# Performance work log

Measured on AMD Instinct MI355X. Metric: run time of the kernel, lower is better.

Reference implementation:

```python
import jax, jax.numpy as jnp
import numpy as np

N, E_RAW, F_IN, H, C = 50000, 800000, 500, 5, 32
HID = H * C  # 160
NEG_GAT = 0.2   # GATConv leaky_relu slope for attention logits
NEG = 0.01      # F.leaky_relu default slope
LN_EPS = 1e-5


def glorot(key, shape):
    fan_in, fan_out = shape[0], shape[-1]
    lim = jnp.sqrt(6.0 / (fan_in + fan_out))
    return jax.random.uniform(key, shape, jnp.float32, -lim, lim)


def setup_inputs() -> dict:
    key = jax.random.key(0)
    ks = jax.random.split(key, 12)
    x = jax.random.normal(ks[0], (N, F_IN), jnp.float32)
    edge_index = jax.random.randint(ks[1], (2, E_RAW), 0, N, jnp.int64)
    return {
        "x": x,
        "edge_index": edge_index,
        "W1": glorot(ks[2], (F_IN, HID)),
        "att1_s": glorot(ks[3], (H, C)),
        "att1_d": glorot(ks[4], (H, C)),
        "b1": jnp.zeros((HID,), jnp.float32),
        "g1": jnp.ones((HID,), jnp.float32),
        "be1": jnp.zeros((HID,), jnp.float32),
        "W2": glorot(ks[5], (HID, HID)),
        "att2_s": glorot(ks[6], (H, C)),
        "att2_d": glorot(ks[7], (H, C)),
        "b2": jnp.zeros((HID,), jnp.float32),
        "Wm": glorot(ks[8], (HID, HID)),
        "bm": jnp.zeros((HID,), jnp.float32),
    }


def add_self_loops(edge_index):
    loops = jnp.arange(N, dtype=edge_index.dtype)
    return jnp.concatenate([edge_index, jnp.stack([loops, loops])], axis=1)


def gat_conv(x, src, dst, W, att_s, att_d, bias):
    # x: [N, Fin] -> per-head transform [N, H, C]
    xl = (x @ W).reshape(N, H, C)
    a_s = jnp.einsum('nhc,hc->nh', xl, att_s)  # [N, H]
    a_d = jnp.einsum('nhc,hc->nh', xl, att_d)
    logits = jax.nn.leaky_relu(a_s[src] + a_d[dst], NEG_GAT)  # [E, H]
    # segment softmax over incoming edges of each dst node
    lmax = jax.ops.segment_max(logits, dst, num_segments=N)
    alpha = jnp.exp(logits - lmax[dst])
    denom = jax.ops.segment_sum(alpha, dst, num_segments=N)
    alpha = alpha / (denom[dst] + 1e-16)
    msg = xl[src] * alpha[:, :, None]  # [E, H, C]
    out = jax.ops.segment_sum(msg, dst, num_segments=N)
    return out.reshape(N, HID) + bias, alpha


def layer_norm(x, g, b):
    mu = jnp.mean(x, axis=-1, keepdims=True)
    var = jnp.mean((x - mu) ** 2, axis=-1, keepdims=True)
    return (x - mu) * jax.lax.rsqrt(var + LN_EPS) * g + b


def reference(x, edge_index, W1, att1_s, att1_d, b1, g1, be1,
              W2, att2_s, att2_d, b2, Wm, bm):
    ei = add_self_loops(edge_index)
    src, dst = ei[0], ei[1]
    h, alpha1 = gat_conv(x, src, dst, W1, att1_s, att1_d, b1)
    h = jax.nn.leaky_relu(h, NEG)
    h = layer_norm(h, g1, be1)  # dropout is identity in eval mode
    h, alpha2 = gat_conv(h, src, dst, W2, att2_s, att2_d, b2)
    h = jax.nn.leaky_relu(h, NEG)
    out = jax.nn.leaky_relu(h @ Wm + bm, NEG)
    return out, alpha1, alpha2
```

## Files before the change

### kernel.cpp

```cpp
#include <hip/hip_runtime.h>

#define N_NODES 50000
#define E_RAW_N 800000
#define E_TOT   850000
#define F_IN_K  500
#define HID     160

using short8 = __attribute__((ext_vector_type(8))) short;
using f32x4  = __attribute__((ext_vector_type(4))) float;

__device__ __forceinline__ float b2f(unsigned short u) {
  union { unsigned int i; float f; } v; v.i = ((unsigned int)u) << 16; return v.f;
}
__device__ __forceinline__ unsigned short f2b(float f) {
  union { float f; unsigned int i; } v; v.f = f;
  unsigned int i = v.i;
  unsigned int lsb = (i >> 16) & 1u;
  i += 0x7fffu + lsb;
  return (unsigned short)(i >> 16);
}

__device__ __forceinline__ float wsum(float x) {
  #pragma unroll
  for (int o = 32; o; o >>= 1) x += __shfl_xor(x, o, 64);
  return x;
}
__device__ __forceinline__ float wmax(float x) {
  #pragma unroll
  for (int o = 32; o; o >>= 1) x = fmaxf(x, __shfl_xor(x, o, 64));
  return x;
}
__device__ __forceinline__ float lrelu2(float x) { return x > 0.f ? x : 0.2f * x; }

__global__ void detect_kernel(const int* __restrict__ ei, int* __restrict__ flag) {
  if (threadIdx.x == 0 && blockIdx.x == 0) {
    int allz = 1;
    for (int i = 1; i < 128; i += 2) if (ei[i] != 0) { allz = 0; break; }
    *flag = allz;
  }
}
__device__ __forceinline__ int edge_src(const int* ei, int wide, int e) {
  return wide ? ei[2 * e] : ei[e];
}
__device__ __forceinline__ int edge_dst(const int* ei, int wide, int e) {
  return wide ? ei[2 * (E_RAW_N + e)] : ei[E_RAW_N + e];
}

__global__ __launch_bounds__(256) void convert_B(const float* __restrict__ B,
                                                 unsigned short* __restrict__ Bt,
                                                 int K, int KPAD) {
  const int i = blockIdx.x * 256 + threadIdx.x;
  if (i >= HID * KPAD) return;
  const int c = i / KPAD, k = i % KPAD;
  const float b = (k < K) ? B[(long)k * HID + c] : 0.f;
  const unsigned short hi = f2b(b);
  Bt[i] = hi;
  Bt[HID * KPAD + i] = f2b(b - b2f(hi));
}

template<int K, int KPAD, int BK, int MODE, int SPLIT>
__global__ __launch_bounds__(256) void gemm_lds(
    const float* __restrict__ A, const unsigned short* __restrict__ Bt,
    float* __restrict__ C, unsigned short* __restrict__ Ch,
    const float* __restrict__ bias,
    const float* __restrict__ att_s, const float* __restrict__ att_d,
    float* __restrict__ a_s, float* __restrict__ a_d)
{
  constexpr int NP = SPLIT ? 2 : 1;
  constexpr int LSTR = BK + 8;
  constexpr int CHUNKS = KPAD / BK;
  constexpr int KSC = BK / 32;
  constexpr int ROWU = BK / 8;
  constexpr int UNITS = NP * HID * ROWU;
  __shared__ __align__(16) unsigned short Bs[NP][HID][LSTR];

  const int t = threadIdx.x;
  const int l = t & 63;
  const int w = t >> 6;
  const int m = l & 15;
  const int kgrp = (l >> 4) * 8;
  const int rbase = blockIdx.x * 64 + w * 16;
  const int arow = (rbase + m < N_NODES) ? rbase + m : N_NODES - 1;
  const float* Arow = A + (long)arow * K;

  f32x4 acc[10];
  #pragma unroll
  for (int i = 0; i < 10; ++i) acc[i] = (f32x4){0.f, 0.f, 0.f, 0.f};

  if constexpr (CHUNKS == 1) {
    float ar[KSC][8];
    #pragma unroll
    for (int ks = 0; ks < KSC; ++ks) {
      const int kb = ks * 32 + kgrp;
      if (kb + 8 <= K) {
        const float4 a0 = *(const float4*)(Arow + kb);
        const float4 a1 = *(const float4*)(Arow + kb + 4);
        ar[ks][0]=a0.x; ar[ks][1]=a0.y; ar[ks][2]=a0.z; ar[ks][3]=a0.w;
        ar[ks][4]=a1.x; ar[ks][5]=a1.y; ar[ks][6]=a1.z; ar[ks][7]=a1.w;
      } else {
        #pragma unroll
        for (int j = 0; j < 8; ++j) ar[ks][j] = (kb + j < K) ? Arow[kb + j] : 0.f;
      }
    }
    for (int u = t; u < UNITS; u += 256) {
      const int p = u / (HID * ROWU);
      const int rem = u % (HID * ROWU);
      const int c = rem / ROWU;
      const int k8 = rem % ROWU;
      const short8 v = *(const short8*)(Bt + (long)p * HID * KPAD + (long)c * KPAD + k8 * 8);
      *(short8*)&Bs[p][c][k8 * 8] = v;
    }
    __syncthreads();
    #pragma unroll
    for (int ks = 0; ks < KSC; ++ks) {
      short8 ah, al;
      #pragma unroll
      for (int j = 0; j < 8; ++j) {
        const unsigned short h = f2b(ar[ks][j]);
        ah[j] = (short)h;
        if (SPLIT) al[j] = (short)f2b(ar[ks][j] - b2f(h));
      }
      #pragma unroll
      for (int ct = 0; ct < 10; ++ct) {
        const short8 bh = *(const short8*)&Bs[0][ct * 16 + m][ks * 32 + kgrp];
        acc[ct] = __builtin_amdgcn_mfma_f32_16x16x32_bf16(ah, bh, acc[ct], 0, 0, 0);
        if (SPLIT) {
          const short8 bl = *(const short8*)&Bs[SPLIT][ct * 16 + m][ks * 32 + kgrp];
          acc[ct] = __builtin_amdgcn_mfma_f32_16x16x32_bf16(ah, bl, acc[ct], 0, 0, 0);
          acc[ct] = __builtin_amdgcn_mfma_f32_16x16x32_bf16(al, bh, acc[ct], 0, 0, 0);
        }
      }
    }
  } else {
    static_assert(UNITS % 256 == 0, "units must tile threads");
    constexpr int UPT = UNITS / 256;
    short8 rb[UPT];
    float ar[KSC][8];

    #pragma unroll
    for (int i = 0; i < UPT; ++i) {
      const int u = i * 256 + t;
      const int p = u / (HID * ROWU);
      const int rem = u % (HID * ROWU);
      const int c = rem / ROWU;
      const int k8 = rem % ROWU;
      rb[i] = *(const short8*)(Bt + (long)p * HID * KPAD + (long)c * KPAD + k8 * 8);
    }
    #pragma unroll
    for (int ks = 0; ks < KSC; ++ks) {
      const int kb = ks * 32 + kgrp;
      const float4 a0 = *(const float4*)(Arow + kb);
      const float4 a1 = *(const float4*)(Arow + kb + 4);
      ar[ks][0]=a0.x; ar[ks][1]=a0.y; ar[ks][2]=a0.z; ar[ks][3]=a0.w;
      ar[ks][4]=a1.x; ar[ks][5]=a1.y; ar[ks][6]=a1.z; ar[ks][7]=a1.w;
    }

    for (int cc = 0; cc < CHUNKS; ++cc) {
      __syncthreads();
      #pragma unroll
      for (int i = 0; i < UPT; ++i) {
        const int u = i * 256 + t;
        const int p = u / (HID * ROWU);
        const int rem = u % (HID * ROWU);
        const int c = rem / ROWU;
        const int k8 = rem % ROWU;
        *(short8*)&Bs[p][c][k8 * 8] = rb[i];
      }
      __syncthreads();
      short8 rb2[UPT];
      float ar2[KSC][8];
      if (cc + 1 < CHUNKS) {
        #pragma unroll
        for (int i = 0; i < UPT; ++i) {
          const int u = i * 256 + t;
          const int p = u / (HID * ROWU);
          const int rem = u % (HID * ROWU);
          const int c = rem / ROWU;
          const int k8 = rem % ROWU;
          rb2[i] = *(const short8*)(Bt + (long)p * HID * KPAD + (long)c * KPAD + (cc + 1) * BK + k8 * 8);
        }
        #pragma unroll
        for (int ks = 0; ks < KSC; ++ks) {
          const int kb = (cc + 1) * BK + ks * 32 + kgrp;
          if (kb + 8 <= K) {
            const float4 a0 = *(const float4*)(Arow + kb);
            const float4 a1 = *(const float4*)(Arow + kb + 4);
            ar2[ks][0]=a0.x; ar2[ks][1]=a0.y; ar2[ks][2]=a0.z; ar2[ks][3]=a0.w;
            ar2[ks][4]=a1.x; ar2[ks][5]=a1.y; ar2[ks][6]=a1.z; ar2[ks][7]=a1.w;
          } else {
            #pragma unroll
            for (int j = 0; j < 8; ++j) ar2[ks][j] = (kb + j < K) ? Arow[kb + j] : 0.f;
          }
        }
        __builtin_amdgcn_sched_barrier(0);
      }
      #pragma unroll
      for (int ks = 0; ks < KSC; ++ks) {
        short8 ah, al;
        #pragma unroll
        for (int j = 0; j < 8; ++j) {
          const unsigned short h = f2b(ar[ks][j]);
          ah[j] = (short)h;
          if (SPLIT) al[j] = (short)f2b(ar[ks][j] - b2f(h));
        }
        #pragma unroll
        for (int ct = 0; ct < 10; ++ct) {
          const short8 bh = *(const short8*)&Bs[0][ct * 16 + m][ks * 32 + kgrp];
          acc[ct] = __builtin_amdgcn_mfma_f32_16x16x32_bf16(ah, bh, acc[ct], 0, 0, 0);
          if (SPLIT) {
            const short8 bl = *(const short8*)&Bs[SPLIT][ct * 16 + m][ks * 32 + kgrp];
            acc[ct] = __builtin_amdgcn_mfma_f32_16x16x32_bf16(ah, bl, acc[ct], 0, 0, 0);
            acc[ct] = __builtin_amdgcn_mfma_f32_16x16x32_bf16(al, bh, acc[ct], 0, 0, 0);
          }
        }
      }
      if (cc + 1 < CHUNKS) {
        #pragma unroll
        for (int i = 0; i < UPT; ++i) rb[i] = rb2[i];
        #pragma unroll
        for (int ks = 0; ks < KSC; ++ks)
          #pragma unroll
          for (int j = 0; j < 8; ++j) ar[ks][j] = ar2[ks][j];
      }
    }
  }

  const int crow0 = rbase + (l >> 4) * 4;

  if (MODE == 2) {
    #pragma unroll
    for (int r = 0; r < 4; ++r) {
      float ps[5], pd[5];
      #pragma unroll
      for (int h = 0; h < 5; ++h) {
        float s = acc[2*h][r]     * att_s[(2*h) * 16 + m]
                + acc[2*h + 1][r] * att_s[(2*h + 1) * 16 + m];
        float d = acc[2*h][r]     * att_d[(2*h) * 16 + m]
                + acc[2*h + 1][r] * att_d[(2*h + 1) * 16 + m];
        #pragma unroll
        for (int o = 1; o < 16; o <<= 1) {
          s += __shfl_xor(s, o, 64);
          d += __shfl_xor(d, o, 64);
        }
        ps[h] = s; pd[h] = d;
      }
      const int crow = crow0 + r;
      if (crow < N_NODES && m < 5) {
        const float vs = m == 0 ? ps[0] : m == 1 ? ps[1] : m == 2 ? ps[2] : m == 3 ? ps[3] : ps[4];
        const float vd = m == 0 ? pd[0] : m == 1 ? pd[1] : m == 2 ? pd[2] : m == 3 ? pd[3] : pd[4];
        a_s[crow * 5 + m] = vs;
        a_d[crow * 5 + m] = vd;
      }
    }
  }

  #pragma unroll
  for (int r = 0; r < 4; ++r) {
    const int crow = crow0 + r;
    if (crow < N_NODES) {
      #pragma unroll
      for (int ct = 0; ct < 10; ++ct) {
        const int col = ct * 16 + m;
        float v = acc[ct][r];
        if (MODE == 1) { v += bias[col]; v = v > 0.f ? v : 0.01f * v; }
        if (MODE == 2) Ch[(long)crow * HID + col] = f2b(v);
        else           C[(long)crow * HID + col] = v;
      }
    }
  }
}

__global__ __launch_bounds__(256) void count_kernel(const int* __restrict__ ei,
    const int* __restrict__ flag, int* __restrict__ deg) {
  const int e = blockIdx.x * 256 + threadIdx.x;
  if (e >= E_TOT) return;
  const int wide = *flag;
  const int d = (e < E_RAW_N) ? edge_dst(ei, wide, e) : (e - E_RAW_N);
  atomicAdd(&deg[d], 1);
}

#define SCAN_CHUNK 49
__global__ __launch_bounds__(1024) void scan_kernel(const int* __restrict__ deg, int* __restrict__ off) {
  __shared__ int wtot[16];
  const int t = threadIdx.x;
  const int lane = t & 63, wid = t >> 6;
  const int base = t * SCAN_CHUNK;
  int local[SCAN_CHUNK];
  int sum = 0;
  #pragma unroll
  for (int i = 0; i < SCAN_CHUNK; ++i) {
    const int idx = base + i;
    const int v = (idx < N_NODES) ? deg[idx] : 0;
    local[i] = sum;
    sum += v;
  }
  int inc = sum;
  #pragma unroll
  for (int o = 1; o < 64; o <<= 1) {
    const int y = __shfl_up(inc, o, 64);
    if (lane >= o) inc += y;
  }
  if (lane == 63) wtot[wid] = inc;
  __syncthreads();
  if (wid == 0 && lane < 16) {
    const int v = wtot[lane];
    int inc2 = v;
    #pragma unroll
    for (int o = 1; o < 16; o <<= 1) {
      const int y = __shfl_up(inc2, o, 64);
      if (lane >= o) inc2 += y;
    }
    wtot[lane] = inc2 - v;
  }
  __syncthreads();
  const int pre = wtot[wid] + (inc - sum);
  #pragma unroll
  for (int i = 0; i < SCAN_CHUNK; ++i) {
    const int idx = base + i;
    if (idx < N_NODES) off[idx] = pre + local[i];
  }
  if (t == 1023) off[N_NODES] = E_TOT;
}

__global__ __launch_bounds__(256) void fill_kernel(const int* __restrict__ ei,
    const int* __restrict__ flag, const int* __restrict__ off,
    int* __restrict__ fillc, int* __restrict__ csr_src, int* __restrict__ csr_eid) {
  const int e = blockIdx.x * 256 + threadIdx.x;
  if (e >= E_TOT) return;
  const int wide = *flag;
  int s, d;
  if (e < E_RAW_N) { s = edge_src(ei, wide, e); d = edge_dst(ei, wide, e); }
  else { s = e - E_RAW_N; d = s; }
  const int p = off[d] + atomicAdd(&fillc[d], 1);
  csr_src[p] = s;
  csr_eid[p] = e;
}

template<int DO_LN>
__global__ __launch_bounds__(256) void node_kernel(
    const int* __restrict__ off_, const int* __restrict__ csr_src, const int* __restrict__ csr_eid,
    const unsigned short* __restrict__ xlh,
    const float* __restrict__ a_s, const float* __restrict__ a_d,
    float* __restrict__ alpha_out,
    const float* __restrict__ bias,
    const float* __restrict__ gamma_, const float* __restrict__ beta_,
    float* __restrict__ hout)
{
  __shared__ int   srcS[4][64];
  __shared__ float alS[4][64][6];

  const int w = threadIdx.x >> 6;
  const int l = threadIdx.x & 63;
  const int n = blockIdx.x * 4 + w;
  if (n >= N_NODES) return;
  const int off = off_[n];
  const int deg = off_[n + 1] - off;

  const float ad0 = a_d[n*5+0], ad1 = a_d[n*5+1], ad2 = a_d[n*5+2], ad3 = a_d[n*5+3], ad4 = a_d[n*5+4];
  const int hA = l >> 4;
  float accx = 0.f, accy = 0.f, accz = 0.f;

  if (deg <= 64) {
    int src = 0, eid = 0;
    float v0 = -1e30f, v1 = -1e30f, v2 = -1e30f, v3 = -1e30f, v4 = -1e30f;
    if (l < deg) {
      src = csr_src[off + l];
      eid = csr_eid[off + l];
      const float* ap = a_s + src * 5;
      v0 = lrelu2(ap[0] + ad0);
      v1 = lrelu2(ap[1] + ad1);
      v2 = lrelu2(ap[2] + ad2);
      v3 = lrelu2(ap[3] + ad3);
      v4 = lrelu2(ap[4] + ad4);
    }
    const float m0 = wmax(v0), m1 = wmax(v1), m2 = wmax(v2), m3 = wmax(v3), m4 = wmax(v4);
    float e0 = 0.f, e1 = 0.f, e2 = 0.f, e3 = 0.f, e4 = 0.f;
    if (l < deg) {
      e0 = __expf(v0 - m0); e1 = __expf(v1 - m1); e2 = __expf(v2 - m2);
      e3 = __expf(v3 - m3); e4 = __expf(v4 - m4);
    }
    const float i0 = 1.f / (wsum(e0) + 1e-16f), i1 = 1.f / (wsum(e1) + 1e-16f),
                i2 = 1.f / (wsum(e2) + 1e-16f), i3 = 1.f / (wsum(e3) + 1e-16f),
                i4 = 1.f / (wsum(e4) + 1e-16f);
    const float a0 = e0 * i0, a1 = e1 * i1, a2 = e2 * i2, a3 = e3 * i3, a4 = e4 * i4;
    if (l < deg) {
      float* aw = alpha_out + (long)eid * 5;
      aw[0] = a0; aw[1] = a1; aw[2] = a2; aw[3] = a3; aw[4] = a4;
    }
    srcS[w][l] = src;
    alS[w][l][0] = a0; alS[w][l][1] = a1; alS[w][l][2] = a2;
    alS[w][l][3] = a3; alS[w][l][4] = a4;

    const int degR = (deg + 3) & ~3;
    const unsigned cx = 2 * l, cz = 128 + l;
    for (int s0 = 0; s0 < degR; s0 += 4) {
      int sr[4]; float aA[4], aB[4];
      #pragma unroll
      for (int j = 0; j < 4; ++j) {
        sr[j] = srcS[w][s0 + j];
        aA[j] = alS[w][s0 + j][hA];
        aB[j] = alS[w][s0 + j][4];
      }
      ushort2 u2[4]; unsigned short z[4];
      #pragma unroll
      for (int j = 0; j < 4; ++j) {
        const unsigned xb = (unsigned)sr[j] * HID;
        u2[j] = *(const ushort2*)(xlh + xb + cx);
        if (l < 32) z[j] = xlh[xb + cz];
      }
      #pragma unroll
      for (int j = 0; j < 4; ++j) {
        accx += b2f(u2[j].x) * aA[j];
        accy += b2f(u2[j].y) * aA[j];
        if (l < 32) accz += b2f(z[j]) * aB[j];
      }
    }
  } else {
    float m0 = -1e30f, m1 = -1e30f, m2 = -1e30f, m3 = -1e30f, m4 = -1e30f;
    for (int s = l; s < deg; s += 64) {
      const float* ap = a_s + csr_src[off + s] * 5;
      m0 = fmaxf(m0, lrelu2(ap[0] + ad0));
      m1 = fmaxf(m1, lrelu2(ap[1] + ad1));
      m2 = fmaxf(m2, lrelu2(ap[2] + ad2));
      m3 = fmaxf(m3, lrelu2(ap[3] + ad3));
      m4 = fmaxf(m4, lrelu2(ap[4] + ad4));
    }
    m0 = wmax(m0); m1 = wmax(m1); m2 = wmax(m2); m3 = wmax(m3); m4 = wmax(m4);
    float s0 = 0.f, s1 = 0.f, s2 = 0.f, s3 = 0.f, s4 = 0.f;
    for (int s = l; s < deg; s += 64) {
      const float* ap = a_s + csr_src[off + s] * 5;
      s0 += __expf(lrelu2(ap[0] + ad0) - m0);
      s1 += __expf(lrelu2(ap[1] + ad1) - m1);
      s2 += __expf(lrelu2(ap[2] + ad2) - m2);
      s3 += __expf(lrelu2(ap[3] + ad3) - m3);
      s4 += __expf(lrelu2(ap[4] + ad4) - m4);
    }
    const float i0 = 1.f / (wsum(s0) + 1e-16f), i1 = 1.f / (wsum(s1) + 1e-16f),
                i2 = 1.f / (wsum(s2) + 1e-16f), i3 = 1.f / (wsum(s3) + 1e-16f),
                i4 = 1.f / (wsum(s4) + 1e-16f);
    const float adA = hA == 0 ? ad0 : hA == 1 ? ad1 : hA == 2 ? ad2 : ad3;
    const float mA  = hA == 0 ? m0  : hA == 1 ? m1  : hA == 2 ? m2  : m3;
    const float iA  = hA == 0 ? i0  : hA == 1 ? i1  : hA == 2 ? i2  : i3;
    float adw = 0.f, mw = 0.f, iw = 0.f;
    if (l < 5) {
      adw = l == 0 ? ad0 : l == 1 ? ad1 : l == 2 ? ad2 : l == 3 ? ad3 : ad4;
      mw  = l == 0 ? m0  : l == 1 ? m1  : l == 2 ? m2  : l == 3 ? m3  : m4;
      iw  = l == 0 ? i0  : l == 1 ? i1  : l == 2 ? i2  : l == 3 ? i3  : i4;
    }
    for (int s = 0; s < deg; ++s) {
      const int p = off + s;
      const int srcs = csr_src[p];
      const float* ap = a_s + srcs * 5;
      const float aA = __expf(lrelu2(ap[hA] + adA) - mA) * iA;
      const long xb = (long)srcs * HID;
      const ushort2 u2 = *(const ushort2*)(xlh + xb + 2 * l);
      accx += b2f(u2.x) * aA;
      accy += b2f(u2.y) * aA;
      if (l < 32) {
        const float aC = __expf(lrelu2(ap[4] + ad4) - m4) * i4;
        accz += b2f(xlh[xb + 128 + l]) * aC;
      }
      if (l < 5) {
        alpha_out[(long)csr_eid[p] * 5 + l] = __expf(lrelu2(ap[l] + adw) - mw) * iw;
      }
    }
  }

  const int c0 = 2 * l, c2 = 128 + l;
  float v0 = accx + bias[c0];     v0 = v0 > 0.f ? v0 : 0.01f * v0;
  float v1 = accy + bias[c0 + 1]; v1 = v1 > 0.f ? v1 : 0.01f * v1;
  float v2 = 0.f;
  if (l < 32) { v2 = accz + bias[c2]; v2 = v2 > 0.f ? v2 : 0.01f * v2; }

  const long hb = (long)n * HID;
  if (DO_LN) {
    const float tot = wsum(v0 + v1 + v2);
    const float mean = tot * (1.f / 160.f);
    const float d0 = v0 - mean, d1 = v1 - mean;
    float sq = d0 * d0 + d1 * d1;
    float d2 = 0.f;
    if (l < 32) { d2 = v2 - mean; sq += d2 * d2; }
    const float var = wsum(sq) * (1.f / 160.f);
    const float rstd = rsqrtf(var + 1e-5f);
    hout[hb + c0]     = d0 * rstd * gamma_[c0]     + beta_[c0];
    hout[hb + c0 + 1] = d1 * rstd * gamma_[c0 + 1] + beta_[c0 + 1];
    if (l < 32) hout[hb + c2] = d2 * rstd * gamma_[c2] + beta_[c2];
  } else {
    hout[hb + c0]     = v0;
    hout[hb + c0 + 1] = v1;
    if (l < 32) hout[hb + c2] = v2;
  }
}

extern "C" void kernel_launch(void* const* d_in, const int* in_sizes, int n_in,
                              void* d_out, int out_size, void* d_ws, size_t ws_size,
                              hipStream_t stream)
{
  const float* x     = (const float*)d_in[0];
  const int*   ei    = (const int*)d_in[1];
  const float* W1    = (const float*)d_in[2];
  const float* att1s = (const float*)d_in[3];
  const float* att1d = (const float*)d_in[4];
  const float* b1    = (const float*)d_in[5];
  const float* g1    = (const float*)d_in[6];
  const float* be1   = (const float*)d_in[7];
  const float* W2    = (const float*)d_in[8];
  const float* att2s = (const float*)d_in[9];
  const float* att2d = (const float*)d_in[10];
  const float* b2    = (const float*)d_in[11];
  const float* Wm    = (const float*)d_in[12];
  const float* bm    = (const float*)d_in[13];

  float* out    = (float*)d_out;
  float* alpha1 = out + (long)N_NODES * HID;
  float* alpha2 = alpha1 + (long)E_TOT * 5;

  char* p = (char*)d_ws;
  auto alloc = [&](size_t bytes) { void* r = (void*)p; p += (bytes + 255) & ~(size_t)255; return r; };
  float* hbuf = (float*)alloc((size_t)N_NODES * HID * 4);
  unsigned short* xlh = (unsigned short*)alloc((size_t)N_NODES * HID * 2);
  float* as_  = (float*)alloc((size_t)N_NODES * 5 * 4);
  float* ad_  = (float*)alloc((size_t)N_NODES * 5 * 4);
  int* deg    = (int*)alloc((size_t)N_NODES * 4);
  int* fillc  = (int*)alloc((size_t)N_NODES * 4);
  int* off    = (int*)alloc((size_t)(N_NODES + 1) * 4);
  int* csrS   = (int*)alloc((size_t)E_TOT * 4);
  int* csrE   = (int*)alloc((size_t)E_TOT * 4);
  int* flag   = (int*)alloc(256);
  unsigned short* Bt1 = (unsigned short*)alloc((size_t)2 * HID * 512 * 2);
  unsigned short* Bt2 = (unsigned short*)alloc((size_t)2 * HID * 160 * 2);
  unsigned short* Btm = (unsigned short*)alloc((size_t)2 * HID * 160 * 2);

  hipMemsetAsync(deg, 0, (size_t)N_NODES * 4, stream);
  hipMemsetAsync(fillc, 0, (size_t)N_NODES * 4, stream);

  detect_kernel<<<1, 64, 0, stream>>>(ei, flag);
  const int EB = (E_TOT + 255) / 256;
  count_kernel<<<EB, 256, 0, stream>>>(ei, flag, deg);
  scan_kernel<<<1, 1024, 0, stream>>>(deg, off);
  fill_kernel<<<EB, 256, 0, stream>>>(ei, flag, off, fillc, csrS, csrE);

  convert_B<<<(HID * 512 + 255) / 256, 256, 0, stream>>>(W1, Bt1, F_IN_K, 512);
  convert_B<<<(HID * 160 + 255) / 256, 256, 0, stream>>>(W2, Bt2, HID, 160);
  convert_B<<<(HID * 160 + 255) / 256, 256, 0, stream>>>(Wm, Btm, HID, 160);

  const int GB = (N_NODES + 63) / 64;

  gemm_lds<F_IN_K, 512, 64, 2, 1><<<GB, 256, 0, stream>>>(x, Bt1, nullptr, xlh, nullptr, att1s, att1d, as_, ad_);
  node_kernel<1><<<N_NODES / 4, 256, 0, stream>>>(off, csrS, csrE, xlh, as_, ad_, alpha1, b1, g1, be1, hbuf);

  gemm_lds<HID, 160, 160, 2, 0><<<GB, 256, 0, stream>>>(hbuf, Bt2, nullptr, xlh, nullptr, att2s, att2d, as_, ad_);
  node_kernel<0><<<N_NODES / 4, 256, 0, stream>>>(off, csrS, csrE, xlh, as_, ad_, alpha2, b2, nullptr, nullptr, hbuf);

  gemm_lds<HID, 160, 160, 1, 0><<<GB, 256, 0, stream>>>(hbuf, Btm, out, nullptr, bm, nullptr, nullptr, nullptr, nullptr);
}
```

Baseline: 441.4 us.

## Store intermediate node features as bf16 and unify pipelined GEMM over K chunks

```diff
diff --git a/kernel.cpp b/kernel.cpp
--- a/kernel.cpp
+++ b/kernel.cpp
@@ -58,20 +58,23 @@
   Bt[HID * KPAD + i] = f2b(b - b2f(hi));
 }
 
-template<int K, int KPAD, int BK, int MODE, int SPLIT>
+template<typename AT, int K, int KPAD, int BK, int MODE, int SPLIT>
 __global__ __launch_bounds__(256) void gemm_lds(
-    const float* __restrict__ A, const unsigned short* __restrict__ Bt,
+    const AT* __restrict__ A, const unsigned short* __restrict__ Bt,
     float* __restrict__ C, unsigned short* __restrict__ Ch,
     const float* __restrict__ bias,
     const float* __restrict__ att_s, const float* __restrict__ att_d,
     float* __restrict__ a_s, float* __restrict__ a_d)
 {
+  constexpr bool AB16 = (sizeof(AT) == 2);
   constexpr int NP = SPLIT ? 2 : 1;
   constexpr int LSTR = BK + 8;
   constexpr int CHUNKS = KPAD / BK;
   constexpr int KSC = BK / 32;
   constexpr int ROWU = BK / 8;
   constexpr int UNITS = NP * HID * ROWU;
+  static_assert(UNITS % 256 == 0, "units must tile threads");
+  constexpr int UPT = UNITS / 256;
   __shared__ __align__(16) unsigned short Bs[NP][HID][LSTR];
 
   const int t = threadIdx.x;
@@ -81,44 +84,86 @@
   const int kgrp = (l >> 4) * 8;
   const int rbase = blockIdx.x * 64 + w * 16;
   const int arow = (rbase + m < N_NODES) ? rbase + m : N_NODES - 1;
-  const float* Arow = A + (long)arow * K;
+  const AT* Arow = A + (long)arow * K;
 
   f32x4 acc[10];
   #pragma unroll
   for (int i = 0; i < 10; ++i) acc[i] = (f32x4){0.f, 0.f, 0.f, 0.f};
 
-  if constexpr (CHUNKS == 1) {
-    float ar[KSC][8];
+  short8 rb[UPT];
+  float  arF[KSC][8], arF2[KSC][8];
+  short8 arS[KSC], arS2[KSC];
+
+  auto loadB = [&](int cc, short8* dst) {
     #pragma unroll
-    for (int ks = 0; ks < KSC; ++ks) {
-      const int kb = ks * 32 + kgrp;
-      if (kb + 8 <= K) {
-        const float4 a0 = *(const float4*)(Arow + kb);
-        const float4 a1 = *(const float4*)(Arow + kb + 4);
-        ar[ks][0]=a0.x; ar[ks][1]=a0.y; ar[ks][2]=a0.z; ar[ks][3]=a0.w;
-        ar[ks][4]=a1.x; ar[ks][5]=a1.y; ar[ks][6]=a1.z; ar[ks][7]=a1.w;
-      } else {
-        #pragma unroll
-        for (int j = 0; j < 8; ++j) ar[ks][j] = (kb + j < K) ? Arow[kb + j] : 0.f;
-      }
-    }
-    for (int u = t; u < UNITS; u += 256) {
+    for (int i = 0; i < UPT; ++i) {
+      const int u = i * 256 + t;
       const int p = u / (HID * ROWU);
       const int rem = u % (HID * ROWU);
       const int c = rem / ROWU;
       const int k8 = rem % ROWU;
-      const short8 v = *(const short8*)(Bt + (long)p * HID * KPAD + (long)c * KPAD + k8 * 8);
-      *(short8*)&Bs[p][c][k8 * 8] = v;
-    }
+      dst[i] = *(const short8*)(Bt + (long)p * HID * KPAD + (long)c * KPAD + cc * BK + k8 * 8);
+    }
+  };
+  auto loadA = [&](int cc, float aF[KSC][8], short8* aS) {
+    #pragma unroll
+    for (int ks = 0; ks < KSC; ++ks) {
+      const int kb = cc * BK + ks * 32 + kgrp;
+      if constexpr (AB16) {
+        short8 v = (short8){0,0,0,0,0,0,0,0};
+        if (kb + 8 <= K) v = *(const short8*)(Arow + kb);
+        else if (kb < K) {
+          #pragma unroll
+          for (int j = 0; j < 8; ++j) v[j] = (kb + j < K) ? (short)Arow[kb + j] : (short)0;
+        }
+        aS[ks] = v;
+      } else {
+        if (kb + 8 <= K) {
+          const float4 a0 = *(const float4*)(Arow + kb);
+          const float4 a1 = *(const float4*)(Arow + kb + 4);
+          aF[ks][0]=a0.x; aF[ks][1]=a0.y; aF[ks][2]=a0.z; aF[ks][3]=a0.w;
+          aF[ks][4]=a1.x; aF[ks][5]=a1.y; aF[ks][6]=a1.z; aF[ks][7]=a1.w;
+        } else {
+          #pragma unroll
+          for (int j = 0; j < 8; ++j) aF[ks][j] = (kb + j < K) ? (float)Arow[kb + j] : 0.f;
+        }
+      }
+    }
+  };
+
+  loadB(0, rb);
+  loadA(0, arF, arS);
+
+  for (int cc = 0; cc < CHUNKS; ++cc) {
     __syncthreads();
+    #pragma unroll
+    for (int i = 0; i < UPT; ++i) {
+      const int u = i * 256 + t;
+      const int p = u / (HID * ROWU);
+      const int rem = u % (HID * ROWU);
+      const int c = rem / ROWU;
+      const int k8 = rem % ROWU;
+      *(short8*)&Bs[p][c][k8 * 8] = rb[i];
+    }
+    __syncthreads();
+    if (cc + 1 < CHUNKS) {
+      loadB(cc + 1, rb);
+      loadA(cc + 1, arF2, arS2);
+      __builtin_amdgcn_sched_barrier(0);
+    }
+    __builtin_amdgcn_s_setprio(1);
     #pragma unroll
     for (int ks = 0; ks < KSC; ++ks) {
       short8 ah, al;
-      #pragma unroll
-      for (int j = 0; j < 8; ++j) {
-        const unsigned short h = f2b(ar[ks][j]);
-        ah[j] = (short)h;
-        if (SPLIT) al[j] = (short)f2b(ar[ks][j] - b2f(h));
+      if constexpr (AB16) {
+        ah = arS[ks];
+      } else {
+        #pragma unroll
+        for (int j = 0; j < 8; ++j) {
+          const unsigned short h = f2b(arF[ks][j]);
+          ah[j] = (short)h;
+          if (SPLIT) al[j] = (short)f2b(arF[ks][j] - b2f(h));
+        }
       }
       #pragma unroll
       for (int ct = 0; ct < 10; ++ct) {
@@ -131,96 +176,15 @@
         }
       }
     }
-  } else {
-    static_assert(UNITS % 256 == 0, "units must tile threads");
-    constexpr int UPT = UNITS / 256;
-    short8 rb[UPT];
-    float ar[KSC][8];
-
-    #pragma unroll
-    for (int i = 0; i < UPT; ++i) {
-      const int u = i * 256 + t;
-      const int p = u / (HID * ROWU);
-      const int rem = u % (HID * ROWU);
-      const int c = rem / ROWU;
-      const int k8 = rem % ROWU;
-      rb[i] = *(const short8*)(Bt + (long)p * HID * KPAD + (long)c * KPAD + k8 * 8);
-    }
-    #pragma unroll
-    for (int ks = 0; ks < KSC; ++ks) {
-      const int kb = ks * 32 + kgrp;
-      const float4 a0 = *(const float4*)(Arow + kb);
-      const float4 a1 = *(const float4*)(Arow + kb + 4);
-      ar[ks][0]=a0.x; ar[ks][1]=a0.y; ar[ks][2]=a0.z; ar[ks][3]=a0.w;
-      ar[ks][4]=a1.x; ar[ks][5]=a1.y; ar[ks][6]=a1.z; ar[ks][7]=a1.w;
-    }
-
-    for (int cc = 0; cc < CHUNKS; ++cc) {
-      __syncthreads();
-      #pragma unroll
-      for (int i = 0; i < UPT; ++i) {
-        const int u = i * 256 + t;
-        const int p = u / (HID * ROWU);
-        const int rem = u % (HID * ROWU);
-        const int c = rem / ROWU;
-        const int k8 = rem % ROWU;
-        *(short8*)&Bs[p][c][k8 * 8] = rb[i];
-      }
-      __syncthreads();
-      short8 rb2[UPT];
-      float ar2[KSC][8];
-      if (cc + 1 < CHUNKS) {
-        #pragma unroll
-        for (int i = 0; i < UPT; ++i) {
-          const int u = i * 256 + t;
-          const int p = u / (HID * ROWU);
-          const int rem = u % (HID * ROWU);
-          const int c = rem / ROWU;
-          const int k8 = rem % ROWU;
-          rb2[i] = *(const short8*)(Bt + (long)p * HID * KPAD + (long)c * KPAD + (cc + 1) * BK + k8 * 8);
+    __builtin_amdgcn_s_setprio(0);
+    if (cc + 1 < CHUNKS) {
+      #pragma unroll
+      for (int ks = 0; ks < KSC; ++ks) {
+        if constexpr (AB16) arS[ks] = arS2[ks];
+        else {
+          #pragma unroll
+          for (int j = 0; j < 8; ++j) arF[ks][j] = arF2[ks][j];
         }
-        #pragma unroll
-        for (int ks = 0; ks < KSC; ++ks) {
-          const int kb = (cc + 1) * BK + ks * 32 + kgrp;
-          if (kb + 8 <= K) {
-            const float4 a0 = *(const float4*)(Arow + kb);
-            const float4 a1 = *(const float4*)(Arow + kb + 4);
-            ar2[ks][0]=a0.x; ar2[ks][1]=a0.y; ar2[ks][2]=a0.z; ar2[ks][3]=a0.w;
-            ar2[ks][4]=a1.x; ar2[ks][5]=a1.y; ar2[ks][6]=a1.z; ar2[ks][7]=a1.w;
-          } else {
-            #pragma unroll
-            for (int j = 0; j < 8; ++j) ar2[ks][j] = (kb + j < K) ? Arow[kb + j] : 0.f;
-          }
-        }
-        __builtin_amdgcn_sched_barrier(0);
-      }
-      #pragma unroll
-      for (int ks = 0; ks < KSC; ++ks) {
-        short8 ah, al;
-        #pragma unroll
-        for (int j = 0; j < 8; ++j) {
-          const unsigned short h = f2b(ar[ks][j]);
-          ah[j] = (short)h;
-          if (SPLIT) al[j] = (short)f2b(ar[ks][j] - b2f(h));
-        }
-        #pragma unroll
-        for (int ct = 0; ct < 10; ++ct) {
-          const short8 bh = *(const short8*)&Bs[0][ct * 16 + m][ks * 32 + kgrp];
-          acc[ct] = __builtin_amdgcn_mfma_f32_16x16x32_bf16(ah, bh, acc[ct], 0, 0, 0);
-          if (SPLIT) {
-            const short8 bl = *(const short8*)&Bs[SPLIT][ct * 16 + m][ks * 32 + kgrp];
-            acc[ct] = __builtin_amdgcn_mfma_f32_16x16x32_bf16(ah, bl, acc[ct], 0, 0, 0);
-            acc[ct] = __builtin_amdgcn_mfma_f32_16x16x32_bf16(al, bh, acc[ct], 0, 0, 0);
-          }
-        }
-      }
-      if (cc + 1 < CHUNKS) {
-        #pragma unroll
-        for (int i = 0; i < UPT; ++i) rb[i] = rb2[i];
-        #pragma unroll
-        for (int ks = 0; ks < KSC; ++ks)
-          #pragma unroll
-          for (int j = 0; j < 8; ++j) ar[ks][j] = ar2[ks][j];
       }
     }
   }
@@ -344,7 +308,7 @@
     float* __restrict__ alpha_out,
     const float* __restrict__ bias,
     const float* __restrict__ gamma_, const float* __restrict__ beta_,
-    float* __restrict__ hout)
+    unsigned short* __restrict__ hout)
 {
   __shared__ int   srcS[4][64];
   __shared__ float alS[4][64][6];
@@ -391,25 +355,25 @@
     alS[w][l][0] = a0; alS[w][l][1] = a1; alS[w][l][2] = a2;
     alS[w][l][3] = a3; alS[w][l][4] = a4;
 
-    const int degR = (deg + 3) & ~3;
+    const int degR = (deg + 7) & ~7;
     const unsigned cx = 2 * l, cz = 128 + l;
-    for (int s0 = 0; s0 < degR; s0 += 4) {
-      int sr[4]; float aA[4], aB[4];
-      #pragma unroll
-      for (int j = 0; j < 4; ++j) {
+    for (int s0 = 0; s0 < degR; s0 += 8) {
+      int sr[8]; float aA[8], aB[8];
+      #pragma unroll
+      for (int j = 0; j < 8; ++j) {
         sr[j] = srcS[w][s0 + j];
         aA[j] = alS[w][s0 + j][hA];
         aB[j] = alS[w][s0 + j][4];
       }
-      ushort2 u2[4]; unsigned short z[4];
-      #pragma unroll
-      for (int j = 0; j < 4; ++j) {
+      ushort2 u2[8]; unsigned short z[8];
+      #pragma unroll
+      for (int j = 0; j < 8; ++j) {
         const unsigned xb = (unsigned)sr[j] * HID;
         u2[j] = *(const ushort2*)(xlh + xb + cx);
         if (l < 32) z[j] = xlh[xb + cz];
       }
       #pragma unroll
-      for (int j = 0; j < 4; ++j) {
+      for (int j = 0; j < 8; ++j) {
         accx += b2f(u2[j].x) * aA[j];
         accy += b2f(u2[j].y) * aA[j];
         if (l < 32) accz += b2f(z[j]) * aB[j];
@@ -482,13 +446,13 @@
     if (l < 32) { d2 = v2 - mean; sq += d2 * d2; }
     const float var = wsum(sq) * (1.f / 160.f);
     const float rstd = rsqrtf(var + 1e-5f);
-    hout[hb + c0]     = d0 * rstd * gamma_[c0]     + beta_[c0];
-    hout[hb + c0 + 1] = d1 * rstd * gamma_[c0 + 1] + beta_[c0 + 1];
-    if (l < 32) hout[hb + c2] = d2 * rstd * gamma_[c2] + beta_[c2];
+    hout[hb + c0]     = f2b(d0 * rstd * gamma_[c0]     + beta_[c0]);
+    hout[hb + c0 + 1] = f2b(d1 * rstd * gamma_[c0 + 1] + beta_[c0 + 1]);
+    if (l < 32) hout[hb + c2] = f2b(d2 * rstd * gamma_[c2] + beta_[c2]);
   } else {
-    hout[hb + c0]     = v0;
-    hout[hb + c0 + 1] = v1;
-    if (l < 32) hout[hb + c2] = v2;
+    hout[hb + c0]     = f2b(v0);
+    hout[hb + c0 + 1] = f2b(v1);
+    if (l < 32) hout[hb + c2] = f2b(v2);
   }
 }
 
@@ -517,8 +481,8 @@
 
   char* p = (char*)d_ws;
   auto alloc = [&](size_t bytes) { void* r = (void*)p; p += (bytes + 255) & ~(size_t)255; return r; };
-  float* hbuf = (float*)alloc((size_t)N_NODES * HID * 4);
-  unsigned short* xlh = (unsigned short*)alloc((size_t)N_NODES * HID * 2);
+  unsigned short* hb16 = (unsigned short*)alloc((size_t)N_NODES * HID * 2);
+  unsigned short* xlh  = (unsigned short*)alloc((size_t)N_NODES * HID * 2);
   float* as_  = (float*)alloc((size_t)N_NODES * 5 * 4);
   float* ad_  = (float*)alloc((size_t)N_NODES * 5 * 4);
   int* deg    = (int*)alloc((size_t)N_NODES * 4);
@@ -528,8 +492,8 @@
   int* csrE   = (int*)alloc((size_t)E_TOT * 4);
   int* flag   = (int*)alloc(256);
   unsigned short* Bt1 = (unsigned short*)alloc((size_t)2 * HID * 512 * 2);
-  unsigned short* Bt2 = (unsigned short*)alloc((size_t)2 * HID * 160 * 2);
-  unsigned short* Btm = (unsigned short*)alloc((size_t)2 * HID * 160 * 2);
+  unsigned short* Bt2 = (unsigned short*)alloc((size_t)2 * HID * 192 * 2);
+  unsigned short* Btm = (unsigned short*)alloc((size_t)2 * HID * 192 * 2);
 
   hipMemsetAsync(deg, 0, (size_t)N_NODES * 4, stream);
   hipMemsetAsync(fillc, 0, (size_t)N_NODES * 4, stream);
@@ -541,16 +505,16 @@
   fill_kernel<<<EB, 256, 0, stream>>>(ei, flag, off, fillc, csrS, csrE);
 
   convert_B<<<(HID * 512 + 255) / 256, 256, 0, stream>>>(W1, Bt1, F_IN_K, 512);
-  convert_B<<<(HID * 160 + 255) / 256, 256, 0, stream>>>(W2, Bt2, HID, 160);
-  convert_B<<<(HID * 160 + 255) / 256, 256, 0, stream>>>(Wm, Btm, HID, 160);
+  convert_B<<<(HID * 192 + 255) / 256, 256, 0, stream>>>(W2, Bt2, HID, 192);
+  convert_B<<<(HID * 192 + 255) / 256, 256, 0, stream>>>(Wm, Btm, HID, 192);
 
   const int GB = (N_NODES + 63) / 64;
 
-  gemm_lds<F_IN_K, 512, 64, 2, 1><<<GB, 256, 0, stream>>>(x, Bt1, nullptr, xlh, nullptr, att1s, att1d, as_, ad_);
-  node_kernel<1><<<N_NODES / 4, 256, 0, stream>>>(off, csrS, csrE, xlh, as_, ad_, alpha1, b1, g1, be1, hbuf);
-
-  gemm_lds<HID, 160, 160, 2, 0><<<GB, 256, 0, stream>>>(hbuf, Bt2, nullptr, xlh, nullptr, att2s, att2d, as_, ad_);
-  node_kernel<0><<<N_NODES / 4, 256, 0, stream>>>(off, csrS, csrE, xlh, as_, ad_, alpha2, b2, nullptr, nullptr, hbuf);
-
-  gemm_lds<HID, 160, 160, 1, 0><<<GB, 256, 0, stream>>>(hbuf, Btm, out, nullptr, bm, nullptr, nullptr, nullptr, nullptr);
-}
+  gemm_lds<float, F_IN_K, 512, 32, 2, 1><<<GB, 256, 0, stream>>>(x, Bt1, nullptr, xlh, nullptr, att1s, att1d, as_, ad_);
+  node_kernel<1><<<N_NODES / 4, 256, 0, stream>>>(off, csrS, csrE, xlh, as_, ad_, alpha1, b1, g1, be1, hb16);
+
+  gemm_lds<unsigned short, HID, 192, 64, 2, 0><<<GB, 256, 0, stream>>>(hb16, Bt2, nullptr, xlh, nullptr, att2s, att2d, as_, ad_);
+  node_kernel<0><<<N_NODES / 4, 256, 0, stream>>>(off, csrS, csrE, xlh, as_, ad_, alpha2, b2, nullptr, nullptr, hb16);
+
+  gemm_lds<unsigned short, HID, 192, 64, 1, 0><<<GB, 256, 0, stream>>>(hb16, Btm, out, nullptr, bm, nullptr, nullptr, nullptr, nullptr);
+}
```

Result: faster. 424.3 us (-3.9%).
